# Kernel optimization log

Hardware: AMD Instinct MI355X
Metric: run time of the kernel (lower is better)

## Reference

```python
import jax, jax.numpy as jnp
import numpy as np
from jax import lax

C = 192; H = W = T = 32; WS = 4; SS = 2; NH = 6; HD = C // NH
N = WS ** 3; NB = 4; HIDDEN = 4 * C; OUT = 192


def _rel_index():
    c = np.stack(np.meshgrid(np.arange(WS), np.arange(WS), np.arange(WS), indexing='ij')).reshape(3, -1)
    r = (c[:, :, None] - c[:, None, :]).transpose(1, 2, 0) + (WS - 1)
    return (r[..., 0] * (2 * WS - 1) ** 2 + r[..., 1] * (2 * WS - 1) + r[..., 2]).astype(np.int32)  # (N,N)


def _attn_mask():
    m = np.zeros((H, W, T), np.float32)
    sl = [slice(0, -WS), slice(-WS, -SS), slice(-SS, None)]
    cnt = 0
    for hs in sl:
        for ws_ in sl:
            for ts in sl:
                m[hs, ws_, ts] = cnt
                cnt += 1
    mw = m.reshape(H // WS, WS, W // WS, WS, T // WS, WS).transpose(0, 2, 4, 1, 3, 5).reshape(-1, N)
    am = mw[:, None, :] - mw[:, :, None]  # (nW,N,N)
    return np.where(am != 0, -100.0, 0.0).astype(np.float32)

_RPI = _rel_index()
_MASK = _attn_mask()


def _ln(x, g, b):
    mu = x.mean(-1, keepdims=True)
    v = ((x - mu) ** 2).mean(-1, keepdims=True)
    return (x - mu) / jnp.sqrt(v + 1e-5) * g + b


def _partition(x):  # (B,H,W,T,C) -> (B*nW,N,C)
    b = x.shape[0]
    x = x.reshape(b, H // WS, WS, W // WS, WS, T // WS, WS, C)
    return x.transpose(0, 1, 3, 5, 2, 4, 6, 7).reshape(-1, N, C)


def _reverse(w, b):  # (B*nW,N,C) -> (B,H,W,T,C)
    x = w.reshape(b, H // WS, W // WS, T // WS, WS, WS, WS, C)
    return x.transpose(0, 1, 4, 2, 5, 3, 6, 7).reshape(b, H, W, T, C)


def _swin_block(xf, shifted, p, mask):
    (n1g, n1b, qw, qb, rp, pw, pb, n2g, n2b, f1w, f1b, f2w, f2b) = p
    b = xf.shape[0]
    shortcut = xf
    h = _ln(xf, n1g, n1b).reshape(b, H, W, T, C)
    if shifted:
        h = jnp.roll(h, (-SS, -SS, -SS), (1, 2, 3))
    wins = _partition(h)  # (b*nW,N,C)
    qkv = (wins @ qw + qb).reshape(-1, N, 3, NH, HD).transpose(2, 0, 3, 1, 4)
    q, k, v = qkv[0], qkv[1], qkv[2]  # (b*nW,NH,N,HD)
    attn = jnp.einsum('bhnd,bhmd->bhnm', q * (HD ** -0.5), k)
    attn = attn + rp[_RPI].transpose(2, 0, 1)[None]  # + rel-pos bias (NH,N,N)
    if shifted:
        nW = mask.shape[0]
        attn = (attn.reshape(b, nW, NH, N, N) + mask[None, :, None]).reshape(-1, NH, N, N)
    attn = jax.nn.softmax(attn, -1)
    o = jnp.einsum('bhnm,bhmd->bhnd', attn, v).transpose(0, 2, 1, 3).reshape(-1, N, C)
    o = o @ pw + pb
    h = _reverse(o, b)
    if shifted:
        h = jnp.roll(h, (SS, SS, SS), (1, 2, 3))
    xf = shortcut + h.reshape(b, -1, C)
    z = _ln(xf, n2g, n2b)
    z = jax.nn.gelu(z @ f1w + f1b, approximate=False) @ f2w + f2b
    return xf + z


def _forward(x, norm1_g, norm1_b, qkv_w, qkv_b, rpb, proj_w, proj_b,
             norm2_g, norm2_b, fc1_w, fc1_b, fc2_w, fc2_b,
             dw_w, dw_b, pw_w, pw_b, bn_g, bn_b):
    b = x.shape[0]
    xf = x.reshape(b, C, -1).transpose(0, 2, 1)  # b (h w t) c
    mask = jnp.asarray(_MASK)
    for i in range(NB):
        p = (norm1_g[i], norm1_b[i], qkv_w[i], qkv_b[i], rpb[i], proj_w[i], proj_b[i],
             norm2_g[i], norm2_b[i], fc1_w[i], fc1_b[i], fc2_w[i], fc2_b[i])
        xf = _swin_block(xf, i % 2 == 1, p, mask)
    y = xf.transpose(0, 2, 1).reshape(b, C, H, W, T)
    # refine: depthwise 3x3x3 + pointwise 1x1x1 conv, eval-mode BN (mean 0, var 1), ReLU
    dn = ('NCDHW', 'OIDHW', 'NCDHW')
    y = lax.conv_general_dilated(y, dw_w, (1, 1, 1), [(1, 1)] * 3,
                                 dimension_numbers=dn, feature_group_count=C) + dw_b.reshape(1, -1, 1, 1, 1)
    y = lax.conv_general_dilated(y, pw_w, (1, 1, 1), [(0, 0)] * 3,
                                 dimension_numbers=dn) + pw_b.reshape(1, -1, 1, 1, 1)
    y = y / jnp.sqrt(1.0 + 1e-5) * bn_g.reshape(1, -1, 1, 1, 1) + bn_b.reshape(1, -1, 1, 1, 1)
    return jax.nn.relu(y)


def setup_inputs() -> dict:
    ks = jax.random.split(jax.random.key(0), 12)
    s = 0.02
    return {
        'x': jax.random.normal(ks[0], (2, C, H, W, T), jnp.float32),
        'norm1_g': jnp.ones((NB, C)), 'norm1_b': jnp.zeros((NB, C)),
        'qkv_w': jax.random.normal(ks[1], (NB, C, 3 * C)) * s, 'qkv_b': jnp.zeros((NB, 3 * C)),
        'rpb': jax.random.normal(ks[2], (NB, (2 * WS - 1) ** 3, NH)) * s,
        'proj_w': jax.random.normal(ks[3], (NB, C, C)) * s, 'proj_b': jnp.zeros((NB, C)),
        'norm2_g': jnp.ones((NB, C)), 'norm2_b': jnp.zeros((NB, C)),
        'fc1_w': jax.random.normal(ks[4], (NB, C, HIDDEN)) * s, 'fc1_b': jnp.zeros((NB, HIDDEN)),
        'fc2_w': jax.random.normal(ks[5], (NB, HIDDEN, C)) * s, 'fc2_b': jnp.zeros((NB, C)),
        'dw_w': jax.random.normal(ks[6], (C, 1, 3, 3, 3)) * 0.1, 'dw_b': jnp.zeros((C,)),
        'pw_w': jax.random.normal(ks[7], (OUT, C, 1, 1, 1)) * 0.05, 'pw_b': jnp.zeros((OUT,)),
        'bn_g': jnp.ones((OUT,)), 'bn_b': jnp.zeros((OUT,)),
    }


def reference(x, norm1_g, norm1_b, qkv_w, qkv_b, rpb, proj_w, proj_b,
              norm2_g, norm2_b, fc1_w, fc1_b, fc2_w, fc2_b,
              dw_w, dw_b, pw_w, pw_b, bn_g, bn_b):
    return _forward(x, norm1_g, norm1_b, qkv_w, qkv_b, rpb, proj_w, proj_b,
                    norm2_g, norm2_b, fc1_w, fc1_b, fc2_w, fc2_b,
                    dw_w, dw_b, pw_w, pw_b, bn_g, bn_b)
```

## Files before the change

### kernel.cpp

```cpp
#include <hip/hip_runtime.h>
#include <hip/hip_bf16.h>

#define DI __device__ __forceinline__

typedef short bf16x8 __attribute__((ext_vector_type(8)));
typedef float f32x4 __attribute__((ext_vector_type(4)));
typedef short s16x4 __attribute__((ext_vector_type(4)));

DI short f2bf(float f) {
    __hip_bfloat16 h = __float2bfloat16(f);
    return *reinterpret_cast<short*>(&h);
}

DI void gload_lds16(const short* gsrc, short* ldst) {
    __builtin_amdgcn_global_load_lds(
        (const __attribute__((address_space(1))) void*)gsrc,
        (__attribute__((address_space(3))) void*)ldst, 16, 0, 0);
}

DI int reg3(int p) { return p < 28 ? 0 : (p < 30 ? 1 : 2); }

__global__ __launch_bounds__(256) void transpose_in(const float* __restrict__ x,
                                                    float* __restrict__ xf) {
    __shared__ float tile[32][33];
    int b = blockIdx.z;
    int c0 = blockIdx.y * 32;
    int l0 = blockIdx.x * 32;
    int tx = threadIdx.x, ty = threadIdx.y;
#pragma unroll
    for (int i = 0; i < 32; i += 8)
        tile[ty + i][tx] = x[(long)(b * 192 + c0 + ty + i) * 32768 + l0 + tx];
    __syncthreads();
#pragma unroll
    for (int i = 0; i < 32; i += 8)
        xf[(long)(b * 32768 + l0 + ty + i) * 192 + c0 + tx] = tile[tx][ty + i];
}

__global__ __launch_bounds__(256) void prep_w(const float* __restrict__ qkv_w,
                                              const float* __restrict__ proj_w,
                                              const float* __restrict__ fc1_w,
                                              const float* __restrict__ fc2_w,
                                              const float* __restrict__ pw_w,
                                              short* __restrict__ wt) {
    int i = blockIdx.x * 256 + threadIdx.x;
    float v;
    if (i < 1769472) {
        int b4 = i / 442368, r = i - b4 * 442368;
        if (r < 110592) { int n = r / 192, k = r - n * 192; v = qkv_w[b4 * 110592 + k * 576 + n]; }
        else if (r < 147456) { int r2 = r - 110592; int n = r2 / 192, k = r2 - n * 192; v = proj_w[b4 * 36864 + k * 192 + n]; }
        else if (r < 294912) { int r2 = r - 147456; int n = r2 / 192, k = r2 - n * 192; v = fc1_w[b4 * 147456 + k * 768 + n]; }
        else { int r2 = r - 294912; int n = r2 / 768, k = r2 - n * 768; v = fc2_w[b4 * 147456 + k * 192 + n]; }
        wt[i] = f2bf(v);
    } else {
        int r = i - 1769472;
        wt[i] = f2bf(pw_w[r]);
    }
}

__global__ __launch_bounds__(256) void qkv_k(const float* __restrict__ XF,
                                             const short* __restrict__ Wg,
                                             const float* __restrict__ bias,
                                             const float* __restrict__ n1g,
                                             const float* __restrict__ n1b,
                                             short* __restrict__ out, int shift) {
    __shared__ short Ws[2][12288];
    const int tid = threadIdx.x;
    const int wv = tid >> 6, lane = tid & 63;
    const int lr = lane & 15, lg = lane >> 4;
    const int mt = ((blockIdx.x & 7) << 6) + (blockIdx.x >> 3);
    const int m0 = mt << 7;

    bf16x8 areg[2][6];
#pragma unroll
    for (int mf = 0; mf < 2; mf++) {
        int row = m0 + (wv << 5) + (mf << 4) + lr;
        int b = row >> 15, r = row & 32767, widx = r >> 6, n = r & 63;
        int wh = widx >> 6, ww = (widx >> 3) & 7, wt = widx & 7;
        int ih = n >> 4, iw = (n >> 2) & 3, it = n & 3;
        int h = ((wh << 2) + ih + shift) & 31;
        int w = ((ww << 2) + iw + shift) & 31;
        int t = ((wt << 2) + it + shift) & 31;
        const float* rp = XF + ((long)(b << 15) + (h << 10) + (w << 5) + t) * 192;
        f32x4 xv[6][2];
        float s = 0.f, sq = 0.f;
#pragma unroll
        for (int kk = 0; kk < 6; kk++)
#pragma unroll
            for (int q = 0; q < 2; q++) {
                xv[kk][q] = *(const f32x4*)(rp + kk * 32 + (lg << 3) + q * 4);
#pragma unroll
                for (int e = 0; e < 4; e++) {
                    s += xv[kk][q][e];
                    sq += xv[kk][q][e] * xv[kk][q][e];
                }
            }
        s += __shfl_xor(s, 16, 64); s += __shfl_xor(s, 32, 64);
        sq += __shfl_xor(sq, 16, 64); sq += __shfl_xor(sq, 32, 64);
        float mu = s * (1.f / 192.f);
        float var = sq * (1.f / 192.f) - mu * mu;
        float rstd = rsqrtf(var + 1e-5f);
#pragma unroll
        for (int kk = 0; kk < 6; kk++) {
            int cb = kk * 32 + (lg << 3);
            f32x4 g0 = *(const f32x4*)(n1g + cb), g1 = *(const f32x4*)(n1g + cb + 4);
            f32x4 b0 = *(const f32x4*)(n1b + cb), b1v = *(const f32x4*)(n1b + cb + 4);
            bf16x8 tt;
#pragma unroll
            for (int e = 0; e < 4; e++) {
                tt[e] = f2bf((xv[kk][0][e] - mu) * rstd * g0[e] + b0[e]);
                tt[e + 4] = f2bf((xv[kk][1][e] - mu) * rstd * g1[e] + b1v[e]);
            }
            areg[mf][kk] = tt;
        }
    }

    auto stage = [&](int jc, int buf) {
#pragma unroll
        for (int q = 0; q < 6; q++) {
            int base = (wv * 6 + q) * 512;
            int E = base + lane * 8;
            int row = E / 192;
            int cb = (E - row * 192) >> 3;
            gload_lds16(Wg + (long)(jc * 64 + row) * 192 + ((cb ^ (row & 7)) << 3),
                        &Ws[buf][base]);
        }
    };

    stage(0, 0);
    __syncthreads();

    for (int j = 0; j < 9; j++) {
        if (j < 8) stage(j + 1, (j + 1) & 1);
        const short* W = Ws[j & 1];
        f32x4 acc[2][4] = {};
#pragma unroll
        for (int kk = 0; kk < 6; kk++) {
            int cb = (kk << 2) + lg;
            bf16x8 wf[4];
#pragma unroll
            for (int nf = 0; nf < 4; nf++) {
                int r = (nf << 4) + lr;
                wf[nf] = *(const bf16x8*)(W + r * 192 + ((cb ^ (r & 7)) << 3));
            }
#pragma unroll
            for (int mf = 0; mf < 2; mf++)
#pragma unroll
                for (int nf = 0; nf < 4; nf++)
                    acc[mf][nf] = __builtin_amdgcn_mfma_f32_16x16x32_bf16(
                        areg[mf][kk], wf[nf], acc[mf][nf], 0, 0, 0);
        }
#pragma unroll
        for (int mf = 0; mf < 2; mf++) {
#pragma unroll
            for (int nf = 0; nf < 4; nf++) {
                int col = j * 64 + (nf << 4) + lr;
                float bv = bias[col];
#pragma unroll
                for (int e = 0; e < 4; e++) {
                    int row = m0 + (wv << 5) + (mf << 4) + (lg << 2) + e;
                    out[(long)row * 576 + col] = f2bf(acc[mf][nf][e] + bv);
                }
            }
        }
        __syncthreads();
    }
}

template <int MODE>
__global__ __launch_bounds__(256) void wk_k(const short* __restrict__ A,
                                            const short* __restrict__ Wg,
                                            const float* __restrict__ bias,
                                            float* __restrict__ resid, float* __restrict__ outF,
                                            const float* __restrict__ bng,
                                            const float* __restrict__ bnb, int shift) {
    __shared__ short Ws[36864];
    const int tid = threadIdx.x;
    const int wv = tid >> 6, lane = tid & 63;
    const int lr = lane & 15, lg = lane >> 4;
    const int mt = ((blockIdx.x & 7) << 6) + (blockIdx.x >> 3);
    const int m0 = mt << 7;

    bf16x8 areg[2][6];
#pragma unroll
    for (int mf = 0; mf < 2; mf++)
#pragma unroll
        for (int kk = 0; kk < 6; kk++)
            areg[mf][kk] = *(const bf16x8*)(A + (long)(m0 + (wv << 5) + (mf << 4) + lr) * 192 + kk * 32 + (lg << 3));

#pragma unroll
    for (int q = 0; q < 18; q++) {
        int base = (wv * 18 + q) * 512;
        int E = base + lane * 8;
        int row = E / 192;
        int cb = (E - row * 192) >> 3;
        gload_lds16(Wg + (long)row * 192 + ((cb ^ (row & 7)) << 3), Ws + base);
    }
    __syncthreads();

    f32x4 acc[2][12] = {};
#pragma unroll
    for (int kk = 0; kk < 6; kk++) {
        int cb = (kk << 2) + lg;
#pragma unroll
        for (int njb = 0; njb < 3; njb++) {
            bf16x8 wf[4];
#pragma unroll
            for (int q = 0; q < 4; q++) {
                int r = ((njb * 4 + q) << 4) + lr;
                wf[q] = *(const bf16x8*)(Ws + r * 192 + ((cb ^ (r & 7)) << 3));
            }
#pragma unroll
            for (int mf = 0; mf < 2; mf++)
#pragma unroll
                for (int q = 0; q < 4; q++)
                    acc[mf][njb * 4 + q] = __builtin_amdgcn_mfma_f32_16x16x32_bf16(
                        areg[mf][kk], wf[q], acc[mf][njb * 4 + q], 0, 0, 0);
        }
    }

#pragma unroll
    for (int mf = 0; mf < 2; mf++) {
        int rbase = m0 + (wv << 5) + (mf << 4) + (lg << 2);
#pragma unroll
        for (int nj = 0; nj < 12; nj++) {
            int col = (nj << 4) + lr;
            float bv = bias[col];
            if (MODE == 4) {
                float sc = 0.9999950000374997f * bng[col];
                float bb = bnb[col];
                f32x4 o;
#pragma unroll
                for (int e = 0; e < 4; e++) {
                    float v = (acc[mf][nj][e] + bv) * sc + bb;
                    o[e] = v > 0.f ? v : 0.f;
                }
                int b = rbase >> 15, l = rbase & 32767;
                *(f32x4*)(outF + ((long)(b * 192 + col) << 15) + l) = o;
            } else {
#pragma unroll
                for (int e = 0; e < 4; e++) {
                    int r = rbase + e;
                    int b = r >> 15, rr = r & 32767, widx = rr >> 6, n = rr & 63;
                    int wh = widx >> 6, ww = (widx >> 3) & 7, wt = widx & 7;
                    int ih = n >> 4, iw = (n >> 2) & 3, it = n & 3;
                    int h = ((wh << 2) + ih + shift) & 31;
                    int w = ((ww << 2) + iw + shift) & 31;
                    int t = ((wt << 2) + it + shift) & 31;
                    long tok = (long)(b << 15) + (h << 10) + (w << 5) + t;
                    resid[tok * 192 + col] += acc[mf][nj][e] + bv;
                }
            }
        }
    }
}

__global__ __launch_bounds__(512, 2) void mlp_k(const float* __restrict__ XF,
                                                const short* __restrict__ W1g,
                                                const short* __restrict__ W2g,
                                                const float* __restrict__ b1,
                                                const float* __restrict__ b2,
                                                const float* __restrict__ n2g,
                                                const float* __restrict__ n2b,
                                                float* __restrict__ resid) {
    __shared__ short Wbuf[2][24576];
    __shared__ short Hs[16384];
    const int tid = threadIdx.x;
    const int wv = tid >> 6, lane = tid & 63;
    const int lr = lane & 15, lg = lane >> 4;
    const int mt = ((blockIdx.x & 7) << 5) + (blockIdx.x >> 3);
    const int m0 = mt << 8;
    short* hw = Hs + (wv << 11);

    bf16x8 areg[2][6];
#pragma unroll
    for (int mf = 0; mf < 2; mf++) {
        const float* rp = XF + (long)(m0 + (wv << 5) + (mf << 4) + lr) * 192;
        f32x4 xv[6][2];
        float s = 0.f, sq = 0.f;
#pragma unroll
        for (int kk = 0; kk < 6; kk++)
#pragma unroll
            for (int q = 0; q < 2; q++) {
                xv[kk][q] = *(const f32x4*)(rp + kk * 32 + (lg << 3) + q * 4);
#pragma unroll
                for (int e = 0; e < 4; e++) {
                    s += xv[kk][q][e];
                    sq += xv[kk][q][e] * xv[kk][q][e];
                }
            }
        s += __shfl_xor(s, 16, 64); s += __shfl_xor(s, 32, 64);
        sq += __shfl_xor(sq, 16, 64); sq += __shfl_xor(sq, 32, 64);
        float mu = s * (1.f / 192.f);
        float var = sq * (1.f / 192.f) - mu * mu;
        float rstd = rsqrtf(var + 1e-5f);
#pragma unroll
        for (int kk = 0; kk < 6; kk++) {
            int cb = kk * 32 + (lg << 3);
            f32x4 g0 = *(const f32x4*)(n2g + cb), g1 = *(const f32x4*)(n2g + cb + 4);
            f32x4 b0 = *(const f32x4*)(n2b + cb), b1v = *(const f32x4*)(n2b + cb + 4);
            bf16x8 t;
#pragma unroll
            for (int e = 0; e < 4; e++) {
                t[e] = f2bf((xv[kk][0][e] - mu) * rstd * g0[e] + b0[e]);
                t[e + 4] = f2bf((xv[kk][1][e] - mu) * rstd * g1[e] + b1v[e]);
            }
            areg[mf][kk] = t;
        }
    }

    auto stage = [&](int jc, int buf) {
#pragma unroll
        for (int q = 0; q < 3; q++) {
            int base = (wv * 3 + q) * 512;
            int E = base + lane * 8;
            int row = E / 192;
            int cb = (E - row * 192) >> 3;
            gload_lds16(W1g + (long)(jc * 64 + row) * 192 + ((cb ^ (row & 7)) << 3),
                        &Wbuf[buf][base]);
        }
#pragma unroll
        for (int q = 0; q < 3; q++) {
            int base = (wv * 3 + q) * 512;
            int E = base + lane * 8;
            int row = E >> 6;
            int cb = (E & 63) >> 3;
            gload_lds16(W2g + (long)row * 768 + jc * 64 + ((cb ^ (row & 7)) << 3),
                        &Wbuf[buf][12288 + base]);
        }
    };

    stage(0, 0);
    __syncthreads();

    f32x4 acc[2][12] = {};

    for (int j = 0; j < 12; j++) {
        if (j < 11) stage(j + 1, (j + 1) & 1);
        const short* W1s = Wbuf[j & 1];
        const short* W2s = Wbuf[j & 1] + 12288;

        f32x4 hacc[4][2] = {};
#pragma unroll
        for (int kk = 0; kk < 6; kk++) {
            int cb = (kk << 2) + lg;
            bf16x8 wf[4];
#pragma unroll
            for (int hf = 0; hf < 4; hf++) {
                int r = (hf << 4) + lr;
                wf[hf] = *(const bf16x8*)(W1s + r * 192 + ((cb ^ (r & 7)) << 3));
            }
#pragma unroll
            for (int hf = 0; hf < 4; hf++)
#pragma unroll
                for (int mf = 0; mf < 2; mf++)
                    hacc[hf][mf] = __builtin_amdgcn_mfma_f32_16x16x32_bf16(
                        wf[hf], areg[mf][kk], hacc[hf][mf], 0, 0, 0);
        }

#pragma unroll
        for (int hf = 0; hf < 4; hf++) {
            f32x4 bv = *(const f32x4*)(b1 + j * 64 + (hf << 4) + (lg << 2));
#pragma unroll
            for (int mf = 0; mf < 2; mf++) {
                s16x4 hv;
#pragma unroll
                for (int e = 0; e < 4; e++) {
                    float v = hacc[hf][mf][e] + bv[e];
                    float inner = fmaf(-0.07135481627f, v * v, -1.595769122f);
                    float eterm = __expf(v * inner);
                    float gl = v * __builtin_amdgcn_rcpf(1.f + eterm);
                    hv[e] = f2bf(gl);
                }
                int Mrow = (mf << 4) + lr;
                int blk = (hf << 1) | (lg >> 1);
                *(s16x4*)(hw + Mrow * 64 + ((blk ^ (Mrow & 7)) << 3) + ((lg & 1) << 2)) = hv;
            }
        }
        asm volatile("s_waitcnt lgkmcnt(0)" ::: "memory");

#pragma unroll
        for (int kk = 0; kk < 2; kk++) {
            int cb = (kk << 2) + lg;
            bf16x8 ah[2], bw[12];
#pragma unroll
            for (int mf = 0; mf < 2; mf++) {
                int r = (mf << 4) + lr;
                ah[mf] = *(const bf16x8*)(hw + r * 64 + ((cb ^ (r & 7)) << 3));
            }
#pragma unroll
            for (int nj = 0; nj < 12; nj++) {
                int r = (nj << 4) + lr;
                bw[nj] = *(const bf16x8*)(W2s + r * 64 + ((cb ^ (r & 7)) << 3));
            }
#pragma unroll
            for (int mf = 0; mf < 2; mf++)
#pragma unroll
                for (int nj = 0; nj < 12; nj++)
                    acc[mf][nj] = __builtin_amdgcn_mfma_f32_16x16x32_bf16(
                        ah[mf], bw[nj], acc[mf][nj], 0, 0, 0);
        }
        __syncthreads();
    }

#pragma unroll
    for (int mf = 0; mf < 2; mf++) {
        int rbase = m0 + (wv << 5) + (mf << 4) + (lg << 2);
#pragma unroll
        for (int nj = 0; nj < 12; nj++) {
            int col = (nj << 4) + lr;
            float bv = b2[col];
#pragma unroll
            for (int e = 0; e < 4; e++) {
                long r = rbase + e;
                resid[r * 192 + col] += acc[mf][nj][e] + bv;
            }
        }
    }
}

__global__ __launch_bounds__(256) void attn_k(const short* __restrict__ qkv,
                                              const float* __restrict__ rpb,
                                              short* __restrict__ o, int shifted) {
    __shared__ short lds[4 * 6144];
    const int wv = threadIdx.x >> 6, lane = threadIdx.x & 63;
    short* vT = lds + wv * 6144;
    short* P = lds + wv * 6144 + 2048;
    const int task = blockIdx.x * 4 + wv;
    const int win = task / 6, head = task - win * 6;
    const int lr = lane & 15, lg = lane >> 4;
    const long qbase = (long)win * 64 * 576 + head * 32;

    bf16x8 aq[4], bk[4];
#pragma unroll
    for (int bi = 0; bi < 4; bi++)
        aq[bi] = *(const bf16x8*)(qkv + qbase + (long)((bi << 4) + lr) * 576 + (lg << 3));
#pragma unroll
    for (int bj = 0; bj < 4; bj++)
        bk[bj] = *(const bf16x8*)(qkv + qbase + 192 + (long)((bj << 4) + lr) * 576 + (lg << 3));
    f32x4 s[4][4] = {};
#pragma unroll
    for (int bi = 0; bi < 4; bi++)
#pragma unroll
        for (int bj = 0; bj < 4; bj++)
            s[bi][bj] = __builtin_amdgcn_mfma_f32_16x16x32_bf16(aq[bi], bk[bj], s[bi][bj], 0, 0, 0);

#pragma unroll
    for (int j = 0; j < 4; j++) {
        bf16x8 vv = *(const bf16x8*)(qkv + qbase + 384 + (long)lane * 576 + (j << 3));
#pragma unroll
        for (int e = 0; e < 8; e++) {
            int d = (j << 3) + e;
            vT[d * 64 + (((lane >> 3) ^ (d & 7)) << 3) + (lane & 7)] = vv[e];
        }
    }

    const float SCALE = 0.17677669529663687f;
    int widx = win & 511;
    int wh = widx >> 6, ww = (widx >> 3) & 7, wt = widx & 7;
    int ihm[4], iwm[4], itm[4], lblm[4];
#pragma unroll
    for (int bj = 0; bj < 4; bj++) {
        int m = (bj << 4) + lr;
        ihm[bj] = m >> 4; iwm[bj] = (m >> 2) & 3; itm[bj] = m & 3;
        lblm[bj] = reg3((wh << 2) + ihm[bj]) * 9 + reg3((ww << 2) + iwm[bj]) * 3 + reg3((wt << 2) + itm[bj]);
    }
#pragma unroll
    for (int bi = 0; bi < 4; bi++) {
#pragma unroll
        for (int e = 0; e < 4; e++) {
            int n = (bi << 4) + (lg << 2) + e;
            int ihn = n >> 4, iwn = (n >> 2) & 3, itn = n & 3;
            int lbln = reg3((wh << 2) + ihn) * 9 + reg3((ww << 2) + iwn) * 3 + reg3((wt << 2) + itn);
#pragma unroll
            for (int bj = 0; bj < 4; bj++) {
                int idx = (ihn - ihm[bj] + 3) * 49 + (iwn - iwm[bj] + 3) * 7 + (itn - itm[bj] + 3);
                float bias = rpb[idx * 6 + head];
                float val = s[bi][bj][e] * SCALE + bias;
                if (shifted && lbln != lblm[bj]) val -= 100.f;
                s[bi][bj][e] = val;
            }
        }
    }

#pragma unroll
    for (int bi = 0; bi < 4; bi++) {
#pragma unroll
        for (int e = 0; e < 4; e++) {
            float mx = s[bi][0][e];
#pragma unroll
            for (int bj = 1; bj < 4; bj++) mx = fmaxf(mx, s[bi][bj][e]);
#pragma unroll
            for (int off = 1; off < 16; off <<= 1) mx = fmaxf(mx, __shfl_xor(mx, off, 64));
            float sm = 0.f;
#pragma unroll
            for (int bj = 0; bj < 4; bj++) {
                float p = __expf(s[bi][bj][e] - mx);
                s[bi][bj][e] = p;
                sm += p;
            }
#pragma unroll
            for (int off = 1; off < 16; off <<= 1) sm += __shfl_xor(sm, off, 64);
            float rinv = 1.f / sm;
            int n = (bi << 4) + (lg << 2) + e;
#pragma unroll
            for (int bj = 0; bj < 4; bj++) {
                int m = (bj << 4) + lr;
                P[n * 64 + (((m >> 3) ^ (n & 7)) << 3) + (m & 7)] = f2bf(s[bi][bj][e] * rinv);
            }
        }
    }

    f32x4 oacc[4][2] = {};
#pragma unroll
    for (int ks = 0; ks < 2; ks++) {
        bf16x8 ap[4], bv2[2];
        int kb = (ks << 2) + lg;
#pragma unroll
        for (int bi = 0; bi < 4; bi++) {
            int r = (bi << 4) + lr;
            ap[bi] = *(const bf16x8*)(P + r * 64 + ((kb ^ (r & 7)) << 3));
        }
#pragma unroll
        for (int nf = 0; nf < 2; nf++) {
            int d = (nf << 4) + lr;
            bv2[nf] = *(const bf16x8*)(vT + d * 64 + ((kb ^ (d & 7)) << 3));
        }
#pragma unroll
        for (int bi = 0; bi < 4; bi++)
#pragma unroll
            for (int nf = 0; nf < 2; nf++)
                oacc[bi][nf] = __builtin_amdgcn_mfma_f32_16x16x32_bf16(ap[bi], bv2[nf], oacc[bi][nf], 0, 0, 0);
    }
#pragma unroll
    for (int bi = 0; bi < 4; bi++)
#pragma unroll
        for (int nf = 0; nf < 2; nf++)
#pragma unroll
            for (int e = 0; e < 4; e++) {
                int n = (bi << 4) + (lg << 2) + e;
                int d = (nf << 4) + lr;
                o[((long)win * 64 + n) * 192 + head * 32 + d] = f2bf(oacc[bi][nf][e]);
            }
}

__global__ __launch_bounds__(192) void dw_k(const float* __restrict__ xf,
                                            const float* __restrict__ w,
                                            const float* __restrict__ db,
                                            short* __restrict__ out) {
    int c = threadIdx.x;
    int blk = blockIdx.x;
    int t0 = (blk & 3) << 3;
    int bhw = blk >> 2;
    int b = bhw >> 10, h = (bhw >> 5) & 31, wq = bhw & 31;

    float wr[27];
#pragma unroll
    for (int k = 0; k < 27; k++) wr[k] = w[c * 27 + k];
    float bias = db[c];
    float acc[8];
#pragma unroll
    for (int j = 0; j < 8; j++) acc[j] = bias;

#pragma unroll
    for (int a = 0; a < 3; a++) {
        int hh = h + a - 1;
        if (hh < 0 || hh > 31) continue;
#pragma unroll
        for (int bb = 0; bb < 3; bb++) {
            int ww = wq + bb - 1;
            if (ww < 0 || ww > 31) continue;
            const float* base = xf + ((long)(b << 15) + (hh << 10) + (ww << 5)) * 192 + c;
            float val[10];
#pragma unroll
            for (int tt = 0; tt < 10; tt++) {
                int t = t0 + tt - 1;
                val[tt] = (t >= 0 && t < 32) ? base[t * 192] : 0.f;
            }
#pragma unroll
            for (int d = 0; d < 3; d++) {
                float wv = wr[a * 9 + bb * 3 + d];
#pragma unroll
                for (int j = 0; j < 8; j++)
                    acc[j] = fmaf(val[j + d], wv, acc[j]);
            }
        }
    }
    long obase = ((long)(b << 15) + (h << 10) + (wq << 5) + t0) * 192 + c;
#pragma unroll
    for (int j = 0; j < 8; j++) out[obase + j * 192] = f2bf(acc[j]);
}

extern "C" void kernel_launch(void* const* d_in, const int* in_sizes, int n_in,
                              void* d_out, int out_size, void* d_ws, size_t ws_size,
                              hipStream_t stream) {
    const float* x      = (const float*)d_in[0];
    const float* n1g    = (const float*)d_in[1];
    const float* n1b    = (const float*)d_in[2];
    const float* qkv_w  = (const float*)d_in[3];
    const float* qkv_b  = (const float*)d_in[4];
    const float* rpb    = (const float*)d_in[5];
    const float* proj_w = (const float*)d_in[6];
    const float* proj_b = (const float*)d_in[7];
    const float* n2g    = (const float*)d_in[8];
    const float* n2b    = (const float*)d_in[9];
    const float* fc1_w  = (const float*)d_in[10];
    const float* fc1_b  = (const float*)d_in[11];
    const float* fc2_w  = (const float*)d_in[12];
    const float* fc2_b  = (const float*)d_in[13];
    const float* dw_w   = (const float*)d_in[14];
    const float* dw_b   = (const float*)d_in[15];
    const float* pw_w   = (const float*)d_in[16];
    const float* pw_b   = (const float*)d_in[17];
    const float* bn_g   = (const float*)d_in[18];
    const float* bn_b   = (const float*)d_in[19];
    float* outF = (float*)d_out;

    char* ws = (char*)d_ws;
    float* XF = (float*)ws;
    short* Abuf = (short*)(ws + 50331648);
    short* Bbuf = (short*)(ws + 150994944);
    short* WT = (short*)(ws + 226492416);

    transpose_in<<<dim3(1024, 6, 2), dim3(32, 8), 0, stream>>>(x, XF);
    prep_w<<<7056, 256, 0, stream>>>(qkv_w, proj_w, fc1_w, fc2_w, pw_w, WT);

    for (int i = 0; i < 4; i++) {
        int shifted = i & 1;
        int shift = shifted ? 2 : 0;
        qkv_k<<<512, 256, 0, stream>>>(XF, WT + (long)i * 442368, qkv_b + i * 576,
                                       n1g + i * 192, n1b + i * 192, Bbuf, shift);
        attn_k<<<1536, 256, 0, stream>>>(Bbuf, rpb + i * 2058, Abuf, shifted);
        wk_k<3><<<512, 256, 0, stream>>>(Abuf, WT + (long)i * 442368 + 110592, proj_b + i * 192,
                                         XF, nullptr, nullptr, nullptr, shift);
        mlp_k<<<256, 512, 0, stream>>>(XF, WT + (long)i * 442368 + 147456,
                                       WT + (long)i * 442368 + 294912,
                                       fc1_b + i * 768, fc2_b + i * 192,
                                       n2g + i * 192, n2b + i * 192, XF);
    }

    dw_k<<<8192, 192, 0, stream>>>(XF, dw_w, dw_b, Abuf);
    wk_k<4><<<512, 256, 0, stream>>>(Abuf, WT + 1769472, pw_b,
                                     nullptr, outF, bn_g, bn_b, 0);
}
```

Baseline: 709.4 us.

## Split MLP kernel across 16 waves with 16 rows per wave

The fused MLP kernel now runs 1024 threads per block, each wave owning 16 token rows instead of 32. Per-wave register state (A fragments, hidden and output accumulators) is halved, and weight staging is spread over twice as many waves. The aim is more latency hiding from having more waves resident per CU. In exchange, each weight fragment read from LDS feeds half as many MFMAs, which raises LDS traffic per FLOP. The launch_bounds(1024,4) request may also force tight register limits or spills.

```diff
diff --git a/kernel.cpp b/kernel.cpp
--- a/kernel.cpp
+++ b/kernel.cpp
@@ -254,14 +254,14 @@
     }
 }
 
-__global__ __launch_bounds__(512, 2) void mlp_k(const float* __restrict__ XF,
-                                                const short* __restrict__ W1g,
-                                                const short* __restrict__ W2g,
-                                                const float* __restrict__ b1,
-                                                const float* __restrict__ b2,
-                                                const float* __restrict__ n2g,
-                                                const float* __restrict__ n2b,
-                                                float* __restrict__ resid) {
+__global__ __launch_bounds__(1024, 4) void mlp_k(const float* __restrict__ XF,
+                                                 const short* __restrict__ W1g,
+                                                 const short* __restrict__ W2g,
+                                                 const float* __restrict__ b1,
+                                                 const float* __restrict__ b2,
+                                                 const float* __restrict__ n2g,
+                                                 const float* __restrict__ n2b,
+                                                 float* __restrict__ resid) {
     __shared__ short Wbuf[2][24576];
     __shared__ short Hs[16384];
     const int tid = threadIdx.x;
@@ -269,12 +269,11 @@
     const int lr = lane & 15, lg = lane >> 4;
     const int mt = ((blockIdx.x & 7) << 5) + (blockIdx.x >> 3);
     const int m0 = mt << 8;
-    short* hw = Hs + (wv << 11);
-
-    bf16x8 areg[2][6];
-#pragma unroll
-    for (int mf = 0; mf < 2; mf++) {
-        const float* rp = XF + (long)(m0 + (wv << 5) + (mf << 4) + lr) * 192;
+    short* hw = Hs + (wv << 10);
+
+    bf16x8 areg[6];
+    {
+        const float* rp = XF + (long)(m0 + (wv << 4) + lr) * 192;
         f32x4 xv[6][2];
         float s = 0.f, sq = 0.f;
 #pragma unroll
@@ -304,42 +303,43 @@
                 t[e] = f2bf((xv[kk][0][e] - mu) * rstd * g0[e] + b0[e]);
                 t[e + 4] = f2bf((xv[kk][1][e] - mu) * rstd * g1[e] + b1v[e]);
             }
-            areg[mf][kk] = t;
+            areg[kk] = t;
         }
     }
 
     auto stage = [&](int jc, int buf) {
 #pragma unroll
         for (int q = 0; q < 3; q++) {
-            int base = (wv * 3 + q) * 512;
-            int E = base + lane * 8;
-            int row = E / 192;
-            int cb = (E - row * 192) >> 3;
-            gload_lds16(W1g + (long)(jc * 64 + row) * 192 + ((cb ^ (row & 7)) << 3),
-                        &Wbuf[buf][base]);
-        }
-#pragma unroll
-        for (int q = 0; q < 3; q++) {
-            int base = (wv * 3 + q) * 512;
-            int E = base + lane * 8;
-            int row = E >> 6;
-            int cb = (E & 63) >> 3;
-            gload_lds16(W2g + (long)row * 768 + jc * 64 + ((cb ^ (row & 7)) << 3),
-                        &Wbuf[buf][12288 + base]);
+            int g = wv * 3 + q;
+            if (g < 24) {
+                int base = g * 512;
+                int E = base + lane * 8;
+                int row = E / 192;
+                int cb = (E - row * 192) >> 3;
+                gload_lds16(W1g + (long)(jc * 64 + row) * 192 + ((cb ^ (row & 7)) << 3),
+                            &Wbuf[buf][base]);
+            } else {
+                int base = (g - 24) * 512;
+                int E = base + lane * 8;
+                int row = E >> 6;
+                int cb = (E & 63) >> 3;
+                gload_lds16(W2g + (long)row * 768 + jc * 64 + ((cb ^ (row & 7)) << 3),
+                            &Wbuf[buf][12288 + base]);
+            }
         }
     };
 
     stage(0, 0);
     __syncthreads();
 
-    f32x4 acc[2][12] = {};
+    f32x4 acc[12] = {};
 
     for (int j = 0; j < 12; j++) {
         if (j < 11) stage(j + 1, (j + 1) & 1);
         const short* W1s = Wbuf[j & 1];
         const short* W2s = Wbuf[j & 1] + 12288;
 
-        f32x4 hacc[4][2] = {};
+        f32x4 hacc[4] = {};
 #pragma unroll
         for (int kk = 0; kk < 6; kk++) {
             int cb = (kk << 2) + lg;
@@ -351,60 +351,47 @@
             }
 #pragma unroll
             for (int hf = 0; hf < 4; hf++)
-#pragma unroll
-                for (int mf = 0; mf < 2; mf++)
-                    hacc[hf][mf] = __builtin_amdgcn_mfma_f32_16x16x32_bf16(
-                        wf[hf], areg[mf][kk], hacc[hf][mf], 0, 0, 0);
+                hacc[hf] = __builtin_amdgcn_mfma_f32_16x16x32_bf16(
+                    wf[hf], areg[kk], hacc[hf], 0, 0, 0);
         }
 
 #pragma unroll
         for (int hf = 0; hf < 4; hf++) {
             f32x4 bv = *(const f32x4*)(b1 + j * 64 + (hf << 4) + (lg << 2));
-#pragma unroll
-            for (int mf = 0; mf < 2; mf++) {
-                s16x4 hv;
-#pragma unroll
-                for (int e = 0; e < 4; e++) {
-                    float v = hacc[hf][mf][e] + bv[e];
-                    float inner = fmaf(-0.07135481627f, v * v, -1.595769122f);
-                    float eterm = __expf(v * inner);
-                    float gl = v * __builtin_amdgcn_rcpf(1.f + eterm);
-                    hv[e] = f2bf(gl);
-                }
-                int Mrow = (mf << 4) + lr;
-                int blk = (hf << 1) | (lg >> 1);
-                *(s16x4*)(hw + Mrow * 64 + ((blk ^ (Mrow & 7)) << 3) + ((lg & 1) << 2)) = hv;
-            }
+            s16x4 hv;
+#pragma unroll
+            for (int e = 0; e < 4; e++) {
+                float v = hacc[hf][e] + bv[e];
+                float inner = fmaf(-0.07135481627f, v * v, -1.595769122f);
+                float eterm = __expf(v * inner);
+                float gl = v * __builtin_amdgcn_rcpf(1.f + eterm);
+                hv[e] = f2bf(gl);
+            }
+            int blk = (hf << 1) | (lg >> 1);
+            *(s16x4*)(hw + lr * 64 + ((blk ^ (lr & 7)) << 3) + ((lg & 1) << 2)) = hv;
         }
         asm volatile("s_waitcnt lgkmcnt(0)" ::: "memory");
 
 #pragma unroll
         for (int kk = 0; kk < 2; kk++) {
             int cb = (kk << 2) + lg;
-            bf16x8 ah[2], bw[12];
-#pragma unroll
-            for (int mf = 0; mf < 2; mf++) {
-                int r = (mf << 4) + lr;
-                ah[mf] = *(const bf16x8*)(hw + r * 64 + ((cb ^ (r & 7)) << 3));
-            }
+            bf16x8 ah, bw[12];
+            ah = *(const bf16x8*)(hw + lr * 64 + ((cb ^ (lr & 7)) << 3));
 #pragma unroll
             for (int nj = 0; nj < 12; nj++) {
                 int r = (nj << 4) + lr;
                 bw[nj] = *(const bf16x8*)(W2s + r * 64 + ((cb ^ (r & 7)) << 3));
             }
 #pragma unroll
-            for (int mf = 0; mf < 2; mf++)
-#pragma unroll
-                for (int nj = 0; nj < 12; nj++)
-                    acc[mf][nj] = __builtin_amdgcn_mfma_f32_16x16x32_bf16(
-                        ah[mf], bw[nj], acc[mf][nj], 0, 0, 0);
+            for (int nj = 0; nj < 12; nj++)
+                acc[nj] = __builtin_amdgcn_mfma_f32_16x16x32_bf16(
+                    ah, bw[nj], acc[nj], 0, 0, 0);
         }
         __syncthreads();
     }
 
-#pragma unroll
-    for (int mf = 0; mf < 2; mf++) {
-        int rbase = m0 + (wv << 5) + (mf << 4) + (lg << 2);
+    {
+        int rbase = m0 + (wv << 4) + (lg << 2);
 #pragma unroll
         for (int nj = 0; nj < 12; nj++) {
             int col = (nj << 4) + lr;
@@ -412,7 +399,7 @@
 #pragma unroll
             for (int e = 0; e < 4; e++) {
                 long r = rbase + e;
-                resid[r * 192 + col] += acc[mf][nj][e] + bv;
+                resid[r * 192 + col] += acc[nj][e] + bv;
             }
         }
     }
@@ -632,10 +619,10 @@
         attn_k<<<1536, 256, 0, stream>>>(Bbuf, rpb + i * 2058, Abuf, shifted);
         wk_k<3><<<512, 256, 0, stream>>>(Abuf, WT + (long)i * 442368 + 110592, proj_b + i * 192,
                                          XF, nullptr, nullptr, nullptr, shift);
-        mlp_k<<<256, 512, 0, stream>>>(XF, WT + (long)i * 442368 + 147456,
-                                       WT + (long)i * 442368 + 294912,
-                                       fc1_b + i * 768, fc2_b + i * 192,
-                                       n2g + i * 192, n2b + i * 192, XF);
+        mlp_k<<<256, 1024, 0, stream>>>(XF, WT + (long)i * 442368 + 147456,
+                                        WT + (long)i * 442368 + 294912,
+                                        fc1_b + i * 768, fc2_b + i * 192,
+                                        n2g + i * 192, n2b + i * 192, XF);
     }
 
     dw_k<<<8192, 192, 0, stream>>>(XF, dw_w, dw_b, Abuf);
```

Result: slower. 818.6 us (+15.4%).

## Split MLP kernel work across wave pairs to halve rows per block

Applied to the files above, without the earlier changes.

Each MLP block now handles 128 rows instead of 256, with pairs of waves sharing a 32-row slab: one wave of each pair computes half of the hidden columns and half of the output columns. The grid doubles to 512 blocks, and per-wave accumulator registers are halved. This adds a block-wide barrier between the GELU write and the second GEMM because hidden tiles are now shared across waves. Each weight chunk is also staged twice as often overall, since there are twice as many blocks, which raises global-to-LDS traffic.

```diff
diff --git a/kernel.cpp b/kernel.cpp
--- a/kernel.cpp
+++ b/kernel.cpp
@@ -263,18 +263,19 @@
                                                 const float* __restrict__ n2b,
                                                 float* __restrict__ resid) {
     __shared__ short Wbuf[2][24576];
-    __shared__ short Hs[16384];
+    __shared__ short Hs[4][2048];
     const int tid = threadIdx.x;
     const int wv = tid >> 6, lane = tid & 63;
     const int lr = lane & 15, lg = lane >> 4;
-    const int mt = ((blockIdx.x & 7) << 5) + (blockIdx.x >> 3);
-    const int m0 = mt << 8;
-    short* hw = Hs + (wv << 11);
+    const int pair = wv >> 1, role = wv & 1;
+    const int mt = ((blockIdx.x & 7) << 6) + (blockIdx.x >> 3);
+    const int m0 = mt << 7;
+    short* hw = &Hs[pair][0];
 
     bf16x8 areg[2][6];
 #pragma unroll
     for (int mf = 0; mf < 2; mf++) {
-        const float* rp = XF + (long)(m0 + (wv << 5) + (mf << 4) + lr) * 192;
+        const float* rp = XF + (long)(m0 + (pair << 5) + (mf << 4) + lr) * 192;
         f32x4 xv[6][2];
         float s = 0.f, sq = 0.f;
 #pragma unroll
@@ -332,40 +333,41 @@
     stage(0, 0);
     __syncthreads();
 
-    f32x4 acc[2][12] = {};
+    f32x4 acc[2][6] = {};
 
     for (int j = 0; j < 12; j++) {
         if (j < 11) stage(j + 1, (j + 1) & 1);
         const short* W1s = Wbuf[j & 1];
         const short* W2s = Wbuf[j & 1] + 12288;
 
-        f32x4 hacc[4][2] = {};
+        f32x4 hacc[2][2] = {};
 #pragma unroll
         for (int kk = 0; kk < 6; kk++) {
             int cb = (kk << 2) + lg;
-            bf16x8 wf[4];
-#pragma unroll
-            for (int hf = 0; hf < 4; hf++) {
-                int r = (hf << 4) + lr;
-                wf[hf] = *(const bf16x8*)(W1s + r * 192 + ((cb ^ (r & 7)) << 3));
-            }
-#pragma unroll
-            for (int hf = 0; hf < 4; hf++)
+            bf16x8 wf[2];
+#pragma unroll
+            for (int q = 0; q < 2; q++) {
+                int r = (((role << 1) + q) << 4) + lr;
+                wf[q] = *(const bf16x8*)(W1s + r * 192 + ((cb ^ (r & 7)) << 3));
+            }
+#pragma unroll
+            for (int q = 0; q < 2; q++)
 #pragma unroll
                 for (int mf = 0; mf < 2; mf++)
-                    hacc[hf][mf] = __builtin_amdgcn_mfma_f32_16x16x32_bf16(
-                        wf[hf], areg[mf][kk], hacc[hf][mf], 0, 0, 0);
-        }
-
-#pragma unroll
-        for (int hf = 0; hf < 4; hf++) {
+                    hacc[q][mf] = __builtin_amdgcn_mfma_f32_16x16x32_bf16(
+                        wf[q], areg[mf][kk], hacc[q][mf], 0, 0, 0);
+        }
+
+#pragma unroll
+        for (int q = 0; q < 2; q++) {
+            int hf = (role << 1) + q;
             f32x4 bv = *(const f32x4*)(b1 + j * 64 + (hf << 4) + (lg << 2));
 #pragma unroll
             for (int mf = 0; mf < 2; mf++) {
                 s16x4 hv;
 #pragma unroll
                 for (int e = 0; e < 4; e++) {
-                    float v = hacc[hf][mf][e] + bv[e];
+                    float v = hacc[q][mf][e] + bv[e];
                     float inner = fmaf(-0.07135481627f, v * v, -1.595769122f);
                     float eterm = __expf(v * inner);
                     float gl = v * __builtin_amdgcn_rcpf(1.f + eterm);
@@ -376,43 +378,43 @@
                 *(s16x4*)(hw + Mrow * 64 + ((blk ^ (Mrow & 7)) << 3) + ((lg & 1) << 2)) = hv;
             }
         }
-        asm volatile("s_waitcnt lgkmcnt(0)" ::: "memory");
+        __syncthreads();
 
 #pragma unroll
         for (int kk = 0; kk < 2; kk++) {
             int cb = (kk << 2) + lg;
-            bf16x8 ah[2], bw[12];
+            bf16x8 ah[2], bw[6];
 #pragma unroll
             for (int mf = 0; mf < 2; mf++) {
                 int r = (mf << 4) + lr;
                 ah[mf] = *(const bf16x8*)(hw + r * 64 + ((cb ^ (r & 7)) << 3));
             }
 #pragma unroll
-            for (int nj = 0; nj < 12; nj++) {
-                int r = (nj << 4) + lr;
-                bw[nj] = *(const bf16x8*)(W2s + r * 64 + ((cb ^ (r & 7)) << 3));
+            for (int nq = 0; nq < 6; nq++) {
+                int r = ((role * 6 + nq) << 4) + lr;
+                bw[nq] = *(const bf16x8*)(W2s + r * 64 + ((cb ^ (r & 7)) << 3));
             }
 #pragma unroll
             for (int mf = 0; mf < 2; mf++)
 #pragma unroll
-                for (int nj = 0; nj < 12; nj++)
-                    acc[mf][nj] = __builtin_amdgcn_mfma_f32_16x16x32_bf16(
-                        ah[mf], bw[nj], acc[mf][nj], 0, 0, 0);
+                for (int nq = 0; nq < 6; nq++)
+                    acc[mf][nq] = __builtin_amdgcn_mfma_f32_16x16x32_bf16(
+                        ah[mf], bw[nq], acc[mf][nq], 0, 0, 0);
         }
         __syncthreads();
     }
 
 #pragma unroll
     for (int mf = 0; mf < 2; mf++) {
-        int rbase = m0 + (wv << 5) + (mf << 4) + (lg << 2);
-#pragma unroll
-        for (int nj = 0; nj < 12; nj++) {
-            int col = (nj << 4) + lr;
+        int rbase = m0 + (pair << 5) + (mf << 4) + (lg << 2);
+#pragma unroll
+        for (int nq = 0; nq < 6; nq++) {
+            int col = ((role * 6 + nq) << 4) + lr;
             float bv = b2[col];
 #pragma unroll
             for (int e = 0; e < 4; e++) {
                 long r = rbase + e;
-                resid[r * 192 + col] += acc[mf][nj][e] + bv;
+                resid[r * 192 + col] += acc[mf][nq][e] + bv;
             }
         }
     }
@@ -632,7 +634,7 @@
         attn_k<<<1536, 256, 0, stream>>>(Bbuf, rpb + i * 2058, Abuf, shifted);
         wk_k<3><<<512, 256, 0, stream>>>(Abuf, WT + (long)i * 442368 + 110592, proj_b + i * 192,
                                          XF, nullptr, nullptr, nullptr, shift);
-        mlp_k<<<256, 512, 0, stream>>>(XF, WT + (long)i * 442368 + 147456,
+        mlp_k<<<512, 512, 0, stream>>>(XF, WT + (long)i * 442368 + 147456,
                                        WT + (long)i * 442368 + 294912,
                                        fc1_b + i * 768, fc2_b + i * 192,
                                        n2g + i * 192, n2b + i * 192, XF);
```

Result: slower. 761.8 us (+7.4%).
